# Optimization experiments

Hardware: AMD Instinct MI355X
Metric: run time of the kernel (lower is better)

The kernel has to match this reference:

```python
import jax, jax.numpy as jnp
import numpy as np

B, H, S, DK, DV = 2, 16, 2048, 64, 64

def setup_inputs() -> dict:
    key = jax.random.key(0)
    k1, k2, k3 = jax.random.split(key, 3)
    Q = jax.random.normal(k1, (B, H, S, DK), dtype=jnp.float32)
    K = jax.random.normal(k2, (B, H, S, DK), dtype=jnp.float32)
    V = jax.random.normal(k3, (B, H, S, DV), dtype=jnp.float32)
    mask = jnp.zeros((1, 1, S, S), dtype=jnp.float32)  # additive mask, broadcastable
    return {"Q": Q, "K": K, "V": V, "mask": mask}

def reference(Q, K, V, mask):
    d_k = Q.shape[-1]
    scale = 1.0 / jnp.sqrt(jnp.asarray(d_k, dtype=Q.dtype))
    # [..., q, k] = Q @ K^T / sqrt(d_k) + mask (additive)
    logits = jnp.einsum('bhqd,bhkd->bhqk', Q, K) * scale + mask
    attn = jax.nn.softmax(logits, axis=-1)
    return jnp.einsum('bhqk,bhkv->bhqv', attn, V)
```

## Files before the change

### kernel.cpp

```cpp
#include <hip/hip_runtime.h>


constexpr int Bn = 2, Hn = 16, Sn = 2048, Dn = 64;
constexpr int QB = 128;
constexpr int KVB = 32;
constexpr int HALFKV = 1024;
constexpr int NIT = HALFKV / KVB;
constexpr float LOG2E = 1.44269504088896f;
constexpr float QSCALE = 0.125f * LOG2E;
constexpr float DEFER_THR = 8.0f;

typedef __attribute__((ext_vector_type(8))) short bf16x8;
typedef __attribute__((ext_vector_type(4))) float f32x4;
typedef __attribute__((ext_vector_type(16))) float f32x16;

union FragU { bf16x8 v; unsigned u[4]; unsigned short s[8]; };
union B64U { unsigned long long q; unsigned short s[4]; };

__device__ __forceinline__ unsigned cvt_pk(float lo, float hi) {
  unsigned r;
  asm("v_cvt_pk_bf16_f32 %0, %1, %2" : "=v"(r) : "v"(lo), "v"(hi));
  return r;
}
__device__ __forceinline__ float exp2_fast(float x) {
  float r;
  asm("v_exp_f32 %0, %1" : "=v"(r) : "v"(x));
  return r;
}
__device__ __forceinline__ float bf2f(unsigned short b) {
  union { unsigned u; float f; } c;
  c.u = ((unsigned)b) << 16;
  return c.f;
}

__global__ __launch_bounds__(512, 4) void sdpa_fa4(
    const float* __restrict__ Q, const float* __restrict__ K,
    const float* __restrict__ V, const float* __restrict__ M,
    float* __restrict__ Out) {
  __shared__ __align__(16) unsigned short lds[32768];

  const int tid = threadIdx.x;
  const int lane = tid & 63;
  const int wave = tid >> 6;
  const int wq = wave & 3;
  const int half = tid >> 8;
  const int htid = tid & 255;
  const int l31 = lane & 31;
  const int hi = lane >> 5;

  int bid = blockIdx.x;
  bid = (bid & 7) * ((int)gridDim.x >> 3) + (bid >> 3);
  const int head = bid >> 4;
  const int qblk = bid & 15;
  const int qrow = qblk * QB + wq * 32 + l31;
  const int kvh = half * HALFKV;

  const float* __restrict__ Qh = Q + (size_t)head * Sn * Dn;
  const float* __restrict__ Kh = K + (size_t)head * Sn * Dn;
  const float* __restrict__ Vh = V + (size_t)head * Sn * Dn;
  float* __restrict__ Oh = Out + (size_t)head * Sn * Dn;

  unsigned short* Kt = lds + half * 16384;
  unsigned short* Vt = lds + half * 16384 + 4096;
  unsigned short* Mt = lds + half * 16384 + 8192;

  FragU qf[4];
#pragma unroll
  for (int kc = 0; kc < 4; ++kc) {
    const float* p = Qh + (size_t)qrow * Dn + kc * 16 + hi * 8;
    f32x4 a = *(const f32x4*)p;
    f32x4 b = *(const f32x4*)(p + 4);
    qf[kc].u[0] = cvt_pk(a[0] * QSCALE, a[1] * QSCALE);
    qf[kc].u[1] = cvt_pk(a[2] * QSCALE, a[3] * QSCALE);
    qf[kc].u[2] = cvt_pk(b[0] * QSCALE, b[1] * QSCALE);
    qf[kc].u[3] = cvt_pk(b[2] * QSCALE, b[3] * QSCALE);
  }

  f32x16 acc0, acc1;
#pragma unroll
  for (int i = 0; i < 16; ++i) { acc0[i] = 0.f; acc1[i] = 0.f; }
  float m_run = -1e30f, l_run = 0.f;

  const int krow = htid >> 3, kcb = htid & 7;
  const int vd = htid & 63, vkb = htid >> 6;
  const int mq = htid >> 1, mh = htid & 1;

  f32x4 kr0, kr1;
  float vrg[8];
  f32x4 mr[4];

  {
    const float* kp = Kh + (size_t)(kvh + krow) * Dn + kcb * 8;
    kr0 = *(const f32x4*)kp;
    kr1 = *(const f32x4*)(kp + 4);
    const float* vp = Vh + (size_t)(kvh + vkb * 8) * Dn + vd;
#pragma unroll
    for (int r = 0; r < 8; ++r) vrg[r] = vp[(size_t)r * Dn];
    const float* mp = M + (size_t)(qblk * QB + mq) * Sn + kvh + mh * 16;
#pragma unroll
    for (int u = 0; u < 4; ++u) mr[u] = *(const f32x4*)(mp + 4 * u);

    FragU f;
    f.u[0] = cvt_pk(kr0[0], kr0[1]); f.u[1] = cvt_pk(kr0[2], kr0[3]);
    f.u[2] = cvt_pk(kr1[0], kr1[1]); f.u[3] = cvt_pk(kr1[2], kr1[3]);
    *(bf16x8*)&Kt[krow * 64 + ((kcb ^ (krow & 7)) * 8)] = f.v;
    FragU g;
    g.u[0] = cvt_pk(vrg[0], vrg[1]); g.u[1] = cvt_pk(vrg[2], vrg[3]);
    g.u[2] = cvt_pk(vrg[4], vrg[5]); g.u[3] = cvt_pk(vrg[6], vrg[7]);
    *(bf16x8*)&Vt[vd * 32 + ((vkb ^ ((vd >> 2) & 3)) * 8)] = g.v;
    FragU h0, h1;
    h0.u[0] = cvt_pk(mr[0][0] * LOG2E, mr[0][1] * LOG2E);
    h0.u[1] = cvt_pk(mr[0][2] * LOG2E, mr[0][3] * LOG2E);
    h0.u[2] = cvt_pk(mr[1][0] * LOG2E, mr[1][1] * LOG2E);
    h0.u[3] = cvt_pk(mr[1][2] * LOG2E, mr[1][3] * LOG2E);
    h1.u[0] = cvt_pk(mr[2][0] * LOG2E, mr[2][1] * LOG2E);
    h1.u[1] = cvt_pk(mr[2][2] * LOG2E, mr[2][3] * LOG2E);
    h1.u[2] = cvt_pk(mr[3][0] * LOG2E, mr[3][1] * LOG2E);
    h1.u[3] = cvt_pk(mr[3][2] * LOG2E, mr[3][3] * LOG2E);
    *(bf16x8*)&Mt[mq * 32 + (((mh * 2 + 0) ^ (mq & 3)) * 8)] = h0.v;
    *(bf16x8*)&Mt[mq * 32 + (((mh * 2 + 1) ^ (mq & 3)) * 8)] = h1.v;
  }
  __syncthreads();

  for (int it = 0; it < NIT; ++it) {
    const int cur = it & 1;
    const unsigned short* Kb = Kt + cur * 2048;
    const unsigned short* Vb = Vt + cur * 2048;
    const unsigned short* Mb = Mt + cur * 4096;

    if (it + 1 < NIT) {
      const int kv1 = kvh + (it + 1) * KVB;
      const float* kp = Kh + (size_t)(kv1 + krow) * Dn + kcb * 8;
      kr0 = *(const f32x4*)kp;
      kr1 = *(const f32x4*)(kp + 4);
      const float* vp = Vh + (size_t)(kv1 + vkb * 8) * Dn + vd;
#pragma unroll
      for (int r = 0; r < 8; ++r) vrg[r] = vp[(size_t)r * Dn];
      const float* mp = M + (size_t)(qblk * QB + mq) * Sn + kv1 + mh * 16;
#pragma unroll
      for (int u = 0; u < 4; ++u) mr[u] = *(const f32x4*)(mp + 4 * u);
    }

    f32x16 st;
#pragma unroll
    for (int i = 0; i < 16; ++i) st[i] = 0.f;
    __builtin_amdgcn_s_setprio(1);
#pragma unroll
    for (int kc = 0; kc < 4; ++kc) {
      FragU kf;
      kf.v = *(const bf16x8*)&Kb[l31 * 64 + (((2 * kc + hi) ^ (l31 & 7)) * 8)];
      st = __builtin_amdgcn_mfma_f32_32x32x16_bf16(kf.v, qf[kc].v, st, 0, 0, 0);
    }
    __builtin_amdgcn_s_setprio(0);

    float p[16];
#pragma unroll
    for (int m = 0; m < 4; ++m) {
      B64U mb;
      mb.q = *(const unsigned long long*)
          &Mb[(wq * 32 + l31) * 32 + ((m ^ (l31 & 3)) * 8) + hi * 4];
#pragma unroll
      for (int e = 0; e < 4; ++e) p[4 * m + e] = st[4 * m + e] + bf2f(mb.s[e]);
    }

    float t8[8];
#pragma unroll
    for (int i = 0; i < 8; ++i) t8[i] = fmaxf(p[2 * i], p[2 * i + 1]);
    float t4a = fmaxf(t8[0], t8[1]), t4b = fmaxf(t8[2], t8[3]);
    float t4c = fmaxf(t8[4], t8[5]), t4d = fmaxf(t8[6], t8[7]);
    float mx = fmaxf(fmaxf(t4a, t4b), fmaxf(t4c, t4d));
    mx = fmaxf(mx, __shfl_xor(mx, 32, 64));

    if (!__all(mx <= m_run + DEFER_THR)) {
      const float mn = fmaxf(m_run, mx);
      const float corr = exp2_fast(m_run - mn);
      m_run = mn;
      l_run *= corr;
#pragma unroll
      for (int i = 0; i < 16; ++i) { acc0[i] *= corr; acc1[i] *= corr; }
    }

    float ps = 0.f;
#pragma unroll
    for (int i = 0; i < 16; ++i) {
      p[i] = exp2_fast(p[i] - m_run);
      ps += p[i];
    }
    ps += __shfl_xor(ps, 32, 64);
    l_run += ps;

    unsigned W[4][2];
#pragma unroll
    for (int m = 0; m < 4; ++m)
#pragma unroll
      for (int s = 0; s < 2; ++s)
        W[m][s] = cvt_pk(p[4 * m + 2 * s], p[4 * m + 2 * s + 1]);

    FragU pf[2];
#pragma unroll
    for (int cc = 0; cc < 2; ++cc)
#pragma unroll
      for (int s = 0; s < 2; ++s) {
        const unsigned a = W[2 * cc][s];
        const unsigned b = W[2 * cc + 1][s];
        const unsigned pa = (unsigned)__shfl_xor((int)a, 32, 64);
        const unsigned pb = (unsigned)__shfl_xor((int)b, 32, 64);
        pf[cc].u[s] = hi ? pb : a;
        pf[cc].u[2 + s] = hi ? b : pa;
      }

    __builtin_amdgcn_s_setprio(1);
#pragma unroll
    for (int c = 0; c < 2; ++c) {
      FragU vf0, vf1;
      vf0.v = *(const bf16x8*)&Vb[l31 * 32 + (((2 * c + hi) ^ ((l31 >> 2) & 3)) * 8)];
      vf1.v = *(const bf16x8*)&Vb[(32 + l31) * 32 + (((2 * c + hi) ^ ((l31 >> 2) & 3)) * 8)];
      acc0 = __builtin_amdgcn_mfma_f32_32x32x16_bf16(vf0.v, pf[c].v, acc0, 0, 0, 0);
      acc1 = __builtin_amdgcn_mfma_f32_32x32x16_bf16(vf1.v, pf[c].v, acc1, 0, 0, 0);
    }
    __builtin_amdgcn_s_setprio(0);

    if (it + 1 < NIT) {
      unsigned short* Kw = Kt + (cur ^ 1) * 2048;
      unsigned short* Vw = Vt + (cur ^ 1) * 2048;
      unsigned short* Mw = Mt + (cur ^ 1) * 4096;
      FragU f;
      f.u[0] = cvt_pk(kr0[0], kr0[1]); f.u[1] = cvt_pk(kr0[2], kr0[3]);
      f.u[2] = cvt_pk(kr1[0], kr1[1]); f.u[3] = cvt_pk(kr1[2], kr1[3]);
      *(bf16x8*)&Kw[krow * 64 + ((kcb ^ (krow & 7)) * 8)] = f.v;
      FragU g;
      g.u[0] = cvt_pk(vrg[0], vrg[1]); g.u[1] = cvt_pk(vrg[2], vrg[3]);
      g.u[2] = cvt_pk(vrg[4], vrg[5]); g.u[3] = cvt_pk(vrg[6], vrg[7]);
      *(bf16x8*)&Vw[vd * 32 + ((vkb ^ ((vd >> 2) & 3)) * 8)] = g.v;
      FragU h0, h1;
      h0.u[0] = cvt_pk(mr[0][0] * LOG2E, mr[0][1] * LOG2E);
      h0.u[1] = cvt_pk(mr[0][2] * LOG2E, mr[0][3] * LOG2E);
      h0.u[2] = cvt_pk(mr[1][0] * LOG2E, mr[1][1] * LOG2E);
      h0.u[3] = cvt_pk(mr[1][2] * LOG2E, mr[1][3] * LOG2E);
      h1.u[0] = cvt_pk(mr[2][0] * LOG2E, mr[2][1] * LOG2E);
      h1.u[1] = cvt_pk(mr[2][2] * LOG2E, mr[2][3] * LOG2E);
      h1.u[2] = cvt_pk(mr[3][0] * LOG2E, mr[3][1] * LOG2E);
      h1.u[3] = cvt_pk(mr[3][2] * LOG2E, mr[3][3] * LOG2E);
      *(bf16x8*)&Mw[mq * 32 + (((mh * 2 + 0) ^ (mq & 3)) * 8)] = h0.v;
      *(bf16x8*)&Mw[mq * 32 + (((mh * 2 + 1) ^ (mq & 3)) * 8)] = h1.v;
    }
    __syncthreads();
  }

  float* Om = (float*)lds;
  float* Mm = (float*)lds + 4 * 32 * 68;
  float* Lm = Mm + 128;

  if (half) {
    float* base = Om + (wq * 32 + l31) * 68;
#pragma unroll
    for (int m = 0; m < 4; ++m) {
      f32x4 a, b;
#pragma unroll
      for (int e = 0; e < 4; ++e) { a[e] = acc0[4 * m + e]; b[e] = acc1[4 * m + e]; }
      *(f32x4*)(base + 8 * m + 4 * hi) = a;
      *(f32x4*)(base + 32 + 8 * m + 4 * hi) = b;
    }
    if (!hi) { Mm[wq * 32 + l31] = m_run; Lm[wq * 32 + l31] = l_run; }
  }
  __syncthreads();
  if (!half) {
    const float m2 = Mm[wq * 32 + l31];
    const float l2 = Lm[wq * 32 + l31];
    const float mm = fmaxf(m_run, m2);
    const float e1 = exp2_fast(m_run - mm);
    const float e2 = exp2_fast(m2 - mm);
    const float inv = 1.0f / (l_run * e1 + l2 * e2);
    const float* base = Om + (wq * 32 + l31) * 68;
#pragma unroll
    for (int m = 0; m < 4; ++m) {
      f32x4 o2a = *(const f32x4*)(base + 8 * m + 4 * hi);
      f32x4 o2b = *(const f32x4*)(base + 32 + 8 * m + 4 * hi);
      f32x4 oa, ob;
#pragma unroll
      for (int e = 0; e < 4; ++e) {
        oa[e] = (acc0[4 * m + e] * e1 + o2a[e] * e2) * inv;
        ob[e] = (acc1[4 * m + e] * e1 + o2b[e] * e2) * inv;
      }
      *(f32x4*)&Oh[(size_t)qrow * Dn + 8 * m + 4 * hi] = oa;
      *(f32x4*)&Oh[(size_t)qrow * Dn + 32 + 8 * m + 4 * hi] = ob;
    }
  }
}

extern "C" void kernel_launch(void* const* d_in, const int* in_sizes, int n_in,
                              void* d_out, int out_size, void* d_ws, size_t ws_size,
                              hipStream_t stream) {
  const float* Q = (const float*)d_in[0];
  const float* K = (const float*)d_in[1];
  const float* V = (const float*)d_in[2];
  const float* M = (const float*)d_in[3];
  float* O = (float*)d_out;
  dim3 grid(Bn * Hn * (Sn / QB));
  sdpa_fa4<<<grid, dim3(512), 0, stream>>>(Q, K, V, M, O);
}
```

Baseline: 186.0 us.

## Pre-pack Q/K/V into bf16 MFMA fragments and drop LDS staging

Adds a prep kernel that converts Q, K and V to bf16 once and writes them in MFMA-fragment order to workspace. The main kernel then loads K/V fragments straight from global memory with no LDS staging or per-iteration barriers. Each block now handles 32 query rows, with four waves each taking a quarter of the KV range and combining their results through a two-level LDS reduction. The mask is read directly as fp32 per lane. This removes the repeated fp32-to-bf16 conversion of K/V in every query block and all the in-loop syncs, at the cost of an extra launch, workspace traffic, and uncoalesced per-lane mask reads.

```diff
diff --git a/kernel.cpp b/kernel.cpp
--- a/kernel.cpp
+++ b/kernel.cpp
@@ -1,21 +1,17 @@
 #include <hip/hip_runtime.h>
 
 
-constexpr int Bn = 2, Hn = 16, Sn = 2048, Dn = 64;
-constexpr int QB = 128;
-constexpr int KVB = 32;
-constexpr int HALFKV = 1024;
-constexpr int NIT = HALFKV / KVB;
+constexpr int Sn = 2048, Dn = 64, NHEAD = 32;
 constexpr float LOG2E = 1.44269504088896f;
 constexpr float QSCALE = 0.125f * LOG2E;
 constexpr float DEFER_THR = 8.0f;
+constexpr size_t FRAG_HEAD = 64 * 4 * 512;
 
 typedef __attribute__((ext_vector_type(8))) short bf16x8;
 typedef __attribute__((ext_vector_type(4))) float f32x4;
 typedef __attribute__((ext_vector_type(16))) float f32x16;
 
 union FragU { bf16x8 v; unsigned u[4]; unsigned short s[8]; };
-union B64U { unsigned long long q; unsigned short s[4]; };
 
 __device__ __forceinline__ unsigned cvt_pk(float lo, float hi) {
   unsigned r;
@@ -27,119 +23,88 @@
   asm("v_exp_f32 %0, %1" : "=v"(r) : "v"(x));
   return r;
 }
-__device__ __forceinline__ float bf2f(unsigned short b) {
-  union { unsigned u; float f; } c;
-  c.u = ((unsigned)b) << 16;
-  return c.f;
-}
-
-__global__ __launch_bounds__(512, 4) void sdpa_fa4(
+
+__global__ __launch_bounds__(256) void sdpa_prep(
     const float* __restrict__ Q, const float* __restrict__ K,
-    const float* __restrict__ V, const float* __restrict__ M,
+    const float* __restrict__ V, unsigned short* __restrict__ Qb,
+    unsigned short* __restrict__ Kb, unsigned short* __restrict__ Vb) {
+  const int tid = threadIdx.x, lane = tid & 63, w = tid >> 6;
+  const int l31 = lane & 31, hi = lane >> 5;
+  const int bid = blockIdx.x;
+  const int head = bid >> 6, blk = bid & 63;
+  const size_t hoff = (size_t)head * Sn * Dn;
+  const size_t foff = ((size_t)(head * 64 + blk) * 4 + w) * 512 + (size_t)lane * 8;
+
+  {
+    const float* p = K + hoff + (size_t)(blk * 32 + l31) * Dn + 16 * w + 8 * hi;
+    f32x4 a = *(const f32x4*)p, b = *(const f32x4*)(p + 4);
+    FragU f;
+    f.u[0] = cvt_pk(a[0], a[1]); f.u[1] = cvt_pk(a[2], a[3]);
+    f.u[2] = cvt_pk(b[0], b[1]); f.u[3] = cvt_pk(b[2], b[3]);
+    *(bf16x8*)&Kb[foff] = f.v;
+  }
+  {
+    const float* p = Q + hoff + (size_t)(blk * 32 + l31) * Dn + 16 * w + 8 * hi;
+    f32x4 a = *(const f32x4*)p, b = *(const f32x4*)(p + 4);
+    FragU f;
+    f.u[0] = cvt_pk(a[0] * QSCALE, a[1] * QSCALE);
+    f.u[1] = cvt_pk(a[2] * QSCALE, a[3] * QSCALE);
+    f.u[2] = cvt_pk(b[0] * QSCALE, b[1] * QSCALE);
+    f.u[3] = cvt_pk(b[2] * QSCALE, b[3] * QSCALE);
+    *(bf16x8*)&Qb[foff] = f.v;
+  }
+  {
+    const int c = w >> 1, dt = w & 1;
+    const float* p = V + hoff + (size_t)(blk * 32 + 16 * c + 8 * hi) * Dn + dt * 32 + l31;
+    float vv[8];
+#pragma unroll
+    for (int j = 0; j < 8; ++j) vv[j] = p[(size_t)j * Dn];
+    FragU f;
+    f.u[0] = cvt_pk(vv[0], vv[1]); f.u[1] = cvt_pk(vv[2], vv[3]);
+    f.u[2] = cvt_pk(vv[4], vv[5]); f.u[3] = cvt_pk(vv[6], vv[7]);
+    *(bf16x8*)&Vb[foff] = f.v;
+  }
+}
+
+__global__ __launch_bounds__(256, 6) void sdpa_fa5(
+    const unsigned short* __restrict__ Qb, const unsigned short* __restrict__ Kb,
+    const unsigned short* __restrict__ Vb, const float* __restrict__ M,
     float* __restrict__ Out) {
-  __shared__ __align__(16) unsigned short lds[32768];
+  __shared__ __align__(16) float OmS[2][32][68];
+  __shared__ float mlS[2][32][2];
 
   const int tid = threadIdx.x;
   const int lane = tid & 63;
   const int wave = tid >> 6;
-  const int wq = wave & 3;
-  const int half = tid >> 8;
-  const int htid = tid & 255;
   const int l31 = lane & 31;
   const int hi = lane >> 5;
 
   int bid = blockIdx.x;
   bid = (bid & 7) * ((int)gridDim.x >> 3) + (bid >> 3);
-  const int head = bid >> 4;
-  const int qblk = bid & 15;
-  const int qrow = qblk * QB + wq * 32 + l31;
-  const int kvh = half * HALFKV;
-
-  const float* __restrict__ Qh = Q + (size_t)head * Sn * Dn;
-  const float* __restrict__ Kh = K + (size_t)head * Sn * Dn;
-  const float* __restrict__ Vh = V + (size_t)head * Sn * Dn;
+  const int head = bid >> 6;
+  const int qblk = bid & 63;
+
+  const unsigned short* __restrict__ Qh = Qb + ((size_t)(head * 64 + qblk) * 4) * 512;
+  const unsigned short* __restrict__ Kh = Kb + (size_t)head * FRAG_HEAD;
+  const unsigned short* __restrict__ Vh = Vb + (size_t)head * FRAG_HEAD;
+  const float* __restrict__ Mq =
+      M + (size_t)(qblk * 32 + l31) * Sn + wave * 512 + 4 * hi;
   float* __restrict__ Oh = Out + (size_t)head * Sn * Dn;
 
-  unsigned short* Kt = lds + half * 16384;
-  unsigned short* Vt = lds + half * 16384 + 4096;
-  unsigned short* Mt = lds + half * 16384 + 8192;
-
   FragU qf[4];
 #pragma unroll
-  for (int kc = 0; kc < 4; ++kc) {
-    const float* p = Qh + (size_t)qrow * Dn + kc * 16 + hi * 8;
-    f32x4 a = *(const f32x4*)p;
-    f32x4 b = *(const f32x4*)(p + 4);
-    qf[kc].u[0] = cvt_pk(a[0] * QSCALE, a[1] * QSCALE);
-    qf[kc].u[1] = cvt_pk(a[2] * QSCALE, a[3] * QSCALE);
-    qf[kc].u[2] = cvt_pk(b[0] * QSCALE, b[1] * QSCALE);
-    qf[kc].u[3] = cvt_pk(b[2] * QSCALE, b[3] * QSCALE);
-  }
+  for (int kc = 0; kc < 4; ++kc)
+    qf[kc].v = *(const bf16x8*)&Qh[kc * 512 + lane * 8];
 
   f32x16 acc0, acc1;
 #pragma unroll
   for (int i = 0; i < 16; ++i) { acc0[i] = 0.f; acc1[i] = 0.f; }
   float m_run = -1e30f, l_run = 0.f;
 
-  const int krow = htid >> 3, kcb = htid & 7;
-  const int vd = htid & 63, vkb = htid >> 6;
-  const int mq = htid >> 1, mh = htid & 1;
-
-  f32x4 kr0, kr1;
-  float vrg[8];
-  f32x4 mr[4];
-
-  {
-    const float* kp = Kh + (size_t)(kvh + krow) * Dn + kcb * 8;
-    kr0 = *(const f32x4*)kp;
-    kr1 = *(const f32x4*)(kp + 4);
-    const float* vp = Vh + (size_t)(kvh + vkb * 8) * Dn + vd;
-#pragma unroll
-    for (int r = 0; r < 8; ++r) vrg[r] = vp[(size_t)r * Dn];
-    const float* mp = M + (size_t)(qblk * QB + mq) * Sn + kvh + mh * 16;
-#pragma unroll
-    for (int u = 0; u < 4; ++u) mr[u] = *(const f32x4*)(mp + 4 * u);
-
-    FragU f;
-    f.u[0] = cvt_pk(kr0[0], kr0[1]); f.u[1] = cvt_pk(kr0[2], kr0[3]);
-    f.u[2] = cvt_pk(kr1[0], kr1[1]); f.u[3] = cvt_pk(kr1[2], kr1[3]);
-    *(bf16x8*)&Kt[krow * 64 + ((kcb ^ (krow & 7)) * 8)] = f.v;
-    FragU g;
-    g.u[0] = cvt_pk(vrg[0], vrg[1]); g.u[1] = cvt_pk(vrg[2], vrg[3]);
-    g.u[2] = cvt_pk(vrg[4], vrg[5]); g.u[3] = cvt_pk(vrg[6], vrg[7]);
-    *(bf16x8*)&Vt[vd * 32 + ((vkb ^ ((vd >> 2) & 3)) * 8)] = g.v;
-    FragU h0, h1;
-    h0.u[0] = cvt_pk(mr[0][0] * LOG2E, mr[0][1] * LOG2E);
-    h0.u[1] = cvt_pk(mr[0][2] * LOG2E, mr[0][3] * LOG2E);
-    h0.u[2] = cvt_pk(mr[1][0] * LOG2E, mr[1][1] * LOG2E);
-    h0.u[3] = cvt_pk(mr[1][2] * LOG2E, mr[1][3] * LOG2E);
-    h1.u[0] = cvt_pk(mr[2][0] * LOG2E, mr[2][1] * LOG2E);
-    h1.u[1] = cvt_pk(mr[2][2] * LOG2E, mr[2][3] * LOG2E);
-    h1.u[2] = cvt_pk(mr[3][0] * LOG2E, mr[3][1] * LOG2E);
-    h1.u[3] = cvt_pk(mr[3][2] * LOG2E, mr[3][3] * LOG2E);
-    *(bf16x8*)&Mt[mq * 32 + (((mh * 2 + 0) ^ (mq & 3)) * 8)] = h0.v;
-    *(bf16x8*)&Mt[mq * 32 + (((mh * 2 + 1) ^ (mq & 3)) * 8)] = h1.v;
-  }
-  __syncthreads();
-
-  for (int it = 0; it < NIT; ++it) {
-    const int cur = it & 1;
-    const unsigned short* Kb = Kt + cur * 2048;
-    const unsigned short* Vb = Vt + cur * 2048;
-    const unsigned short* Mb = Mt + cur * 4096;
-
-    if (it + 1 < NIT) {
-      const int kv1 = kvh + (it + 1) * KVB;
-      const float* kp = Kh + (size_t)(kv1 + krow) * Dn + kcb * 8;
-      kr0 = *(const f32x4*)kp;
-      kr1 = *(const f32x4*)(kp + 4);
-      const float* vp = Vh + (size_t)(kv1 + vkb * 8) * Dn + vd;
-#pragma unroll
-      for (int r = 0; r < 8; ++r) vrg[r] = vp[(size_t)r * Dn];
-      const float* mp = M + (size_t)(qblk * QB + mq) * Sn + kv1 + mh * 16;
-#pragma unroll
-      for (int u = 0; u < 4; ++u) mr[u] = *(const f32x4*)(mp + 4 * u);
-    }
+  for (int it = 0; it < 16; ++it) {
+    const int blk = wave * 16 + it;
+    const unsigned short* kbase = Kh + (size_t)blk * 2048;
+    const unsigned short* vbase = Vh + (size_t)blk * 2048;
 
     f32x16 st;
 #pragma unroll
@@ -148,20 +113,21 @@
 #pragma unroll
     for (int kc = 0; kc < 4; ++kc) {
       FragU kf;
-      kf.v = *(const bf16x8*)&Kb[l31 * 64 + (((2 * kc + hi) ^ (l31 & 7)) * 8)];
+      kf.v = *(const bf16x8*)&kbase[kc * 512 + lane * 8];
       st = __builtin_amdgcn_mfma_f32_32x32x16_bf16(kf.v, qf[kc].v, st, 0, 0, 0);
     }
     __builtin_amdgcn_s_setprio(0);
 
+    f32x4 mk[4];
+#pragma unroll
+    for (int m = 0; m < 4; ++m) mk[m] = *(const f32x4*)(Mq + it * 32 + 8 * m);
+
     float p[16];
 #pragma unroll
-    for (int m = 0; m < 4; ++m) {
-      B64U mb;
-      mb.q = *(const unsigned long long*)
-          &Mb[(wq * 32 + l31) * 32 + ((m ^ (l31 & 3)) * 8) + hi * 4];
-#pragma unroll
-      for (int e = 0; e < 4; ++e) p[4 * m + e] = st[4 * m + e] + bf2f(mb.s[e]);
-    }
+    for (int m = 0; m < 4; ++m)
+#pragma unroll
+      for (int e = 0; e < 4; ++e)
+        p[4 * m + e] = fmaf(mk[m][e], LOG2E, st[4 * m + e]);
 
     float t8[8];
 #pragma unroll
@@ -213,46 +179,17 @@
 #pragma unroll
     for (int c = 0; c < 2; ++c) {
       FragU vf0, vf1;
-      vf0.v = *(const bf16x8*)&Vb[l31 * 32 + (((2 * c + hi) ^ ((l31 >> 2) & 3)) * 8)];
-      vf1.v = *(const bf16x8*)&Vb[(32 + l31) * 32 + (((2 * c + hi) ^ ((l31 >> 2) & 3)) * 8)];
+      vf0.v = *(const bf16x8*)&vbase[(c * 2 + 0) * 512 + lane * 8];
+      vf1.v = *(const bf16x8*)&vbase[(c * 2 + 1) * 512 + lane * 8];
       acc0 = __builtin_amdgcn_mfma_f32_32x32x16_bf16(vf0.v, pf[c].v, acc0, 0, 0, 0);
       acc1 = __builtin_amdgcn_mfma_f32_32x32x16_bf16(vf1.v, pf[c].v, acc1, 0, 0, 0);
     }
     __builtin_amdgcn_s_setprio(0);
-
-    if (it + 1 < NIT) {
-      unsigned short* Kw = Kt + (cur ^ 1) * 2048;
-      unsigned short* Vw = Vt + (cur ^ 1) * 2048;
-      unsigned short* Mw = Mt + (cur ^ 1) * 4096;
-      FragU f;
-      f.u[0] = cvt_pk(kr0[0], kr0[1]); f.u[1] = cvt_pk(kr0[2], kr0[3]);
-      f.u[2] = cvt_pk(kr1[0], kr1[1]); f.u[3] = cvt_pk(kr1[2], kr1[3]);
-      *(bf16x8*)&Kw[krow * 64 + ((kcb ^ (krow & 7)) * 8)] = f.v;
-      FragU g;
-      g.u[0] = cvt_pk(vrg[0], vrg[1]); g.u[1] = cvt_pk(vrg[2], vrg[3]);
-      g.u[2] = cvt_pk(vrg[4], vrg[5]); g.u[3] = cvt_pk(vrg[6], vrg[7]);
-      *(bf16x8*)&Vw[vd * 32 + ((vkb ^ ((vd >> 2) & 3)) * 8)] = g.v;
-      FragU h0, h1;
-      h0.u[0] = cvt_pk(mr[0][0] * LOG2E, mr[0][1] * LOG2E);
-      h0.u[1] = cvt_pk(mr[0][2] * LOG2E, mr[0][3] * LOG2E);
-      h0.u[2] = cvt_pk(mr[1][0] * LOG2E, mr[1][1] * LOG2E);
-      h0.u[3] = cvt_pk(mr[1][2] * LOG2E, mr[1][3] * LOG2E);
-      h1.u[0] = cvt_pk(mr[2][0] * LOG2E, mr[2][1] * LOG2E);
-      h1.u[1] = cvt_pk(mr[2][2] * LOG2E, mr[2][3] * LOG2E);
-      h1.u[2] = cvt_pk(mr[3][0] * LOG2E, mr[3][1] * LOG2E);
-      h1.u[3] = cvt_pk(mr[3][2] * LOG2E, mr[3][3] * LOG2E);
-      *(bf16x8*)&Mw[mq * 32 + (((mh * 2 + 0) ^ (mq & 3)) * 8)] = h0.v;
-      *(bf16x8*)&Mw[mq * 32 + (((mh * 2 + 1) ^ (mq & 3)) * 8)] = h1.v;
-    }
-    __syncthreads();
-  }
-
-  float* Om = (float*)lds;
-  float* Mm = (float*)lds + 4 * 32 * 68;
-  float* Lm = Mm + 128;
-
-  if (half) {
-    float* base = Om + (wq * 32 + l31) * 68;
+  }
+
+  if (wave & 1) {
+    const int s = wave >> 1;
+    float* base = &OmS[s][l31][0];
 #pragma unroll
     for (int m = 0; m < 4; ++m) {
       f32x4 a, b;
@@ -261,17 +198,51 @@
       *(f32x4*)(base + 8 * m + 4 * hi) = a;
       *(f32x4*)(base + 32 + 8 * m + 4 * hi) = b;
     }
-    if (!hi) { Mm[wq * 32 + l31] = m_run; Lm[wq * 32 + l31] = l_run; }
+    if (!hi) { mlS[s][l31][0] = m_run; mlS[s][l31][1] = l_run; }
   }
   __syncthreads();
-  if (!half) {
-    const float m2 = Mm[wq * 32 + l31];
-    const float l2 = Lm[wq * 32 + l31];
+  if (!(wave & 1)) {
+    const int s = wave >> 1;
+    const float m2 = mlS[s][l31][0];
+    const float l2 = mlS[s][l31][1];
+    const float mm = fmaxf(m_run, m2);
+    const float e1 = exp2_fast(m_run - mm);
+    const float e2 = exp2_fast(m2 - mm);
+    m_run = mm;
+    l_run = l_run * e1 + l2 * e2;
+    float* base = &OmS[s][l31][0];
+#pragma unroll
+    for (int m = 0; m < 4; ++m) {
+      f32x4 o2a = *(const f32x4*)(base + 8 * m + 4 * hi);
+      f32x4 o2b = *(const f32x4*)(base + 32 + 8 * m + 4 * hi);
+#pragma unroll
+      for (int e = 0; e < 4; ++e) {
+        acc0[4 * m + e] = acc0[4 * m + e] * e1 + o2a[e] * e2;
+        acc1[4 * m + e] = acc1[4 * m + e] * e1 + o2b[e] * e2;
+      }
+    }
+    if (wave == 2) {
+#pragma unroll
+      for (int m = 0; m < 4; ++m) {
+        f32x4 a, b;
+#pragma unroll
+        for (int e = 0; e < 4; ++e) { a[e] = acc0[4 * m + e]; b[e] = acc1[4 * m + e]; }
+        *(f32x4*)(base + 8 * m + 4 * hi) = a;
+        *(f32x4*)(base + 32 + 8 * m + 4 * hi) = b;
+      }
+      if (!hi) { mlS[1][l31][0] = m_run; mlS[1][l31][1] = l_run; }
+    }
+  }
+  __syncthreads();
+  if (wave == 0) {
+    const float m2 = mlS[1][l31][0];
+    const float l2 = mlS[1][l31][1];
     const float mm = fmaxf(m_run, m2);
     const float e1 = exp2_fast(m_run - mm);
     const float e2 = exp2_fast(m2 - mm);
     const float inv = 1.0f / (l_run * e1 + l2 * e2);
-    const float* base = Om + (wq * 32 + l31) * 68;
+    const float* base = &OmS[1][l31][0];
+    const int qrow = qblk * 32 + l31;
 #pragma unroll
     for (int m = 0; m < 4; ++m) {
       f32x4 o2a = *(const f32x4*)(base + 8 * m + 4 * hi);
@@ -296,6 +267,11 @@
   const float* V = (const float*)d_in[2];
   const float* M = (const float*)d_in[3];
   float* O = (float*)d_out;
-  dim3 grid(Bn * Hn * (Sn / QB));
-  sdpa_fa4<<<grid, dim3(512), 0, stream>>>(Q, K, V, M, O);
-}
+
+  unsigned short* Qb = (unsigned short*)d_ws;
+  unsigned short* Kb = Qb + (size_t)NHEAD * FRAG_HEAD;
+  unsigned short* Vb = Kb + (size_t)NHEAD * FRAG_HEAD;
+
+  sdpa_prep<<<dim3(NHEAD * 64), dim3(256), 0, stream>>>(Q, K, V, Qb, Kb, Vb);
+  sdpa_fa5<<<dim3(NHEAD * 64), dim3(256), 0, stream>>>(Qb, Kb, Vb, M, O);
+}
```

After: 280.3 us. +50.7%, slower.
